# Kernel tuning notes

Measured on AMD Instinct MI355X. Metric: run time of the kernel, lower is better.

Reference implementation:

```python
import jax, jax.numpy as jnp
import numpy as np

HID = 1024
NH = 16
HD = HID // NH  # 64
RANK = 16
B, L = 2, 2048


def setup_inputs() -> dict:
    key = jax.random.key(0)
    ks = jax.random.split(key, 9)
    s = 0.02
    return {
        "x": jax.random.normal(ks[0], (B, L, HID), dtype=jnp.float32),
        "Wq": jax.random.normal(ks[1], (HID, HID), dtype=jnp.float32) * s,
        "Wk": jax.random.normal(ks[2], (HID, HID), dtype=jnp.float32) * s,
        "Wv": jax.random.normal(ks[3], (HID, HID), dtype=jnp.float32) * s,
        "Wg": jax.random.normal(ks[4], (HID, HID), dtype=jnp.float32) * s,
        "Wgk1": jax.random.normal(ks[5], (HID, RANK), dtype=jnp.float32) * s,
        "Wgk2": jax.random.normal(ks[6], (RANK, HID), dtype=jnp.float32) * s,
        "bgk2": jnp.zeros((HID,), dtype=jnp.float32),
        "gamma": jnp.ones((HID,), dtype=jnp.float32),
        "beta": jnp.zeros((HID,), dtype=jnp.float32),
        "Wout": jax.random.normal(ks[7], (HID, HID), dtype=jnp.float32) * s,
    }


def reference(x, Wq, Wk, Wv, Wg, Wgk1, Wgk2, bgk2, gamma, beta, Wout):
    Bb, Ll, Hid = x.shape
    H, Dh = NH, HD
    # projections -> [B, L, H, Dh]
    q = (x @ Wq).reshape(Bb, Ll, H, Dh)
    k = (x @ Wk).reshape(Bb, Ll, H, Dh)
    v = (x @ Wv).reshape(Bb, Ll, H, Dh)
    gk = (jax.nn.log_sigmoid((x @ Wgk1) @ Wgk2 + bgk2) / 16.0).reshape(Bb, Ll, H, Dh)

    # time-major for scan: [L, B, H, Dh]
    qT = jnp.transpose(q, (1, 0, 2, 3))
    kT = jnp.transpose(k, (1, 0, 2, 3))
    vT = jnp.transpose(v, (1, 0, 2, 3))
    gT = jnp.transpose(gk, (1, 0, 2, 3))

    def step(state, inp):
        qt, kt, vt, gt = inp  # each [B, H, Dh]
        gate = jnp.exp(gt)
        # state[b,h,v_dim,k_dim]; gate applied along v_dim (matches torch code)
        state = state * gate[..., None] + vt[..., None] * kt[..., None, :]
        out_t = jnp.einsum('bhvk,bhk->bhv', state, qt)
        return state, out_t

    state0 = jnp.zeros((Bb, H, Dh, Dh), dtype=x.dtype)
    _, outs = jax.lax.scan(step, state0, (qT, kT, vT, gT))  # outs: [L, B, H, Dh]
    out = jnp.transpose(outs, (1, 0, 2, 3)).reshape(Bb, Ll, Hid)

    # LayerNorm over total_dim
    mu = out.mean(-1, keepdims=True)
    var = out.var(-1, keepdims=True)
    out = (out - mu) / jnp.sqrt(var + 1e-5) * gamma + beta

    # output gate + projection (dropout = identity in eval)
    out = out * jax.nn.silu(x @ Wg)
    return out @ Wout
```

## Files before the change

### kernel.cpp

```cpp
#include <hip/hip_runtime.h>
#include <cstdint>
#include <cstddef>

#define HIDS 1024
#define NHEAD 16
#define HDIM 64
#define LSEQ 2048
#define BBATCH 2
#define NROW (BBATCH * LSEQ)
#define CHUNK 64
#define NCHUNK (LSEQ / CHUNK)
#define RANK 16

typedef short short8 __attribute__((ext_vector_type(8)));
typedef float floatx4 __attribute__((ext_vector_type(4)));

__device__ __forceinline__ ushort f2bf(float f) {
  uint32_t u = __float_as_uint(f);
  uint32_t r = (u + 0x7fffu + ((u >> 16) & 1u)) >> 16;
  return (ushort)r;
}
__device__ __forceinline__ float bf2f(ushort u) {
  return __uint_as_float(((uint32_t)u) << 16);
}
__device__ __forceinline__ float logsig16(float z) {
  return (fminf(z, 0.f) - __logf(1.f + __expf(-fabsf(z)))) * (1.f / 16.f);
}

__device__ __forceinline__ void async_copy16(const void* g, void* l) {
  __builtin_amdgcn_global_load_lds(
      (const __attribute__((address_space(1))) void*)g,
      (__attribute__((address_space(3))) void*)l, 16, 0, 0);
}

__global__ __launch_bounds__(256) void prep_kernel(
    const float* __restrict__ x, ushort* __restrict__ xbf,
    const float* __restrict__ W0, const float* __restrict__ W1,
    const float* __restrict__ W2, const float* __restrict__ W3,
    const float* __restrict__ W4, ushort* __restrict__ T0,
    ushort* __restrict__ T1, ushort* __restrict__ T2, ushort* __restrict__ T3,
    ushort* __restrict__ T4, const float* __restrict__ Wgk1,
    const float* __restrict__ Wgk2, ushort* __restrict__ Wte) {
  __shared__ float sbuf[64 * 65];
  const int bid = blockIdx.x;
  const int tid = threadIdx.x;

  if (bid < 4096) {
    const int i = bid * 256 + tid;
    float4 f = *(const float4*)(x + (size_t)i * 4);
    ushort4 o;
    o.x = f2bf(f.x); o.y = f2bf(f.y); o.z = f2bf(f.z); o.w = f2bf(f.w);
    *(ushort4*)(xbf + (size_t)i * 4) = o;
  } else if (bid < 5376) {
    const int w = bid - 4096;
    const int z = w >> 8, rem = w & 255;
    const float* W = (z == 0) ? W0 : (z == 1) ? W1 : (z == 2) ? W2
                     : (z == 3) ? W3 : W4;
    ushort* T = (z == 0) ? T0 : (z == 1) ? T1 : (z == 2) ? T2
                : (z == 3) ? T3 : T4;
    const int k0 = (rem >> 4) * 64, n0 = (rem & 15) * 64;
    const int r = tid >> 2, c4 = (tid & 3) * 16;
#pragma unroll
    for (int i = 0; i < 4; ++i) {
      float4 f = *(const float4*)(W + (size_t)(k0 + r) * HIDS + n0 + c4 + i * 4);
      sbuf[r * 65 + c4 + i * 4 + 0] = f.x;
      sbuf[r * 65 + c4 + i * 4 + 1] = f.y;
      sbuf[r * 65 + c4 + i * 4 + 2] = f.z;
      sbuf[r * 65 + c4 + i * 4 + 3] = f.w;
    }
    __syncthreads();
    const int n = tid >> 2, kc = (tid & 3) * 16;
#pragma unroll
    for (int i = 0; i < 4; ++i) {
      int kk = kc + i * 4;
      ushort4 o;
      o.x = f2bf(sbuf[(kk + 0) * 65 + n]);
      o.y = f2bf(sbuf[(kk + 1) * 65 + n]);
      o.z = f2bf(sbuf[(kk + 2) * 65 + n]);
      o.w = f2bf(sbuf[(kk + 3) * 65 + n]);
      *(ushort4*)(T + (size_t)(n0 + n) * HIDS + k0 + kk) = o;
    }
  } else {
    const int rem = bid - 5376;
    const int n0 = (rem & 15) * 64, k0 = (rem >> 4) * 64;
    float* sW1 = sbuf;
    float* sW2 = sbuf + 64 * 17;
    {
      const int kl = tid >> 2, r4 = (tid & 3) * 4;
      float4 f = *(const float4*)(Wgk1 + (size_t)(k0 + kl) * RANK + r4);
      sW1[kl * 17 + r4] = f.x; sW1[kl * 17 + r4 + 1] = f.y;
      sW1[kl * 17 + r4 + 2] = f.z; sW1[kl * 17 + r4 + 3] = f.w;
      const int rr = tid >> 4, nl = (tid & 15) * 4;
      float4 g = *(const float4*)(Wgk2 + (size_t)rr * HIDS + n0 + nl);
      sW2[rr * 65 + nl] = g.x; sW2[rr * 65 + nl + 1] = g.y;
      sW2[rr * 65 + nl + 2] = g.z; sW2[rr * 65 + nl + 3] = g.w;
    }
    __syncthreads();
    const int nl = tid & 63, kq = (tid >> 6) * 16;
    float w2[16];
#pragma unroll
    for (int r = 0; r < 16; ++r) w2[r] = sW2[r * 65 + nl];
    ushort ob[16];
#pragma unroll
    for (int i = 0; i < 16; ++i) {
      float s = 0.f;
#pragma unroll
      for (int r = 0; r < 16; ++r) s = fmaf(sW1[(kq + i) * 17 + r], w2[r], s);
      ob[i] = f2bf(s);
    }
#pragma unroll
    for (int i = 0; i < 2; ++i)
      *(short8*)(Wte + (size_t)(n0 + nl) * HIDS + k0 + kq + i * 8) =
          *(short8*)&ob[i * 8];
  }
}

__global__ __launch_bounds__(256) void proj5_kernel(
    const ushort* __restrict__ xbf, const ushort* __restrict__ Wtq,
    const ushort* __restrict__ Wtk, const ushort* __restrict__ Wtv,
    const ushort* __restrict__ Wtg, const ushort* __restrict__ Wte,
    ushort* __restrict__ qb, ushort* __restrict__ kb, ushort* __restrict__ vb,
    ushort* __restrict__ gb, ushort* __restrict__ zb) {
  const int bxz = blockIdx.x;
  const int z = bxz % 5;
  const int bx = bxz / 5;
  const ushort* Bt = (z == 0) ? Wtq : (z == 1) ? Wtk : (z == 2) ? Wtv
                     : (z == 3) ? Wtg : Wte;
  ushort* C = (z == 0) ? qb : (z == 1) ? kb : (z == 2) ? vb : (z == 3) ? gb : zb;
  __shared__ ushort As[2][128 * 32];
  __shared__ ushort Bs[2][128 * 32];
  const int tid = threadIdx.x;
  const int wave = tid >> 6, lane = tid & 63;
  const int wm = (wave >> 1) * 64, wn = (wave & 1) * 64;
  const int bm = blockIdx.y * 128, bn = bx * 128;
  const int lrow = tid >> 2;
  const int lk8 = ((((tid & 3) - ((tid >> 3) & 3)) & 3)) * 8;
  const ushort* Ag = xbf + (size_t)(bm + lrow) * HIDS + lk8;
  const ushort* Bg = Bt + (size_t)(bn + lrow) * HIDS + lk8;
  char* A0 = (char*)&As[0][0] + tid * 16;
  char* A1 = (char*)&As[1][0] + tid * 16;
  char* B0 = (char*)&Bs[0][0] + tid * 16;
  char* B1 = (char*)&Bs[1][0] + tid * 16;

  floatx4 acc[4][4];
#pragma unroll
  for (int i = 0; i < 4; ++i)
#pragma unroll
    for (int j = 0; j < 4; ++j) acc[i][j] = (floatx4){0.f, 0.f, 0.f, 0.f};

  const int fm = lane & 15, quad = lane >> 4;
  const int sq8 = ((quad + (fm >> 1)) & 3) * 8;

  for (int k0 = 0; k0 < HIDS; k0 += 64) {
    __syncthreads();
    async_copy16(Ag + k0, A0);
    async_copy16(Ag + (size_t)64 * HIDS + k0, A0 + 4096);
    async_copy16(Ag + k0 + 32, A1);
    async_copy16(Ag + (size_t)64 * HIDS + k0 + 32, A1 + 4096);
    async_copy16(Bg + k0, B0);
    async_copy16(Bg + (size_t)64 * HIDS + k0, B0 + 4096);
    async_copy16(Bg + k0 + 32, B1);
    async_copy16(Bg + (size_t)64 * HIDS + k0 + 32, B1 + 4096);
    __syncthreads();

#pragma unroll
    for (int ks = 0; ks < 2; ++ks) {
      short8 af[4], bfr[4];
#pragma unroll
      for (int i = 0; i < 4; ++i)
        af[i] = *(const short8*)&As[ks][(wm + i * 16 + fm) * 32 + sq8];
#pragma unroll
      for (int j = 0; j < 4; ++j)
        bfr[j] = *(const short8*)&Bs[ks][(wn + j * 16 + fm) * 32 + sq8];
#pragma unroll
      for (int i = 0; i < 4; ++i)
#pragma unroll
        for (int j = 0; j < 4; ++j)
          acc[i][j] = __builtin_amdgcn_mfma_f32_16x16x32_bf16(af[i], bfr[j],
                                                              acc[i][j], 0, 0, 0);
    }
  }

#pragma unroll
  for (int i = 0; i < 4; ++i) {
    const int row0 = bm + wm + i * 16 + quad * 4;
#pragma unroll
    for (int j = 0; j < 4; ++j) {
      const int col = bn + wn + j * 16 + fm;
#pragma unroll
      for (int r = 0; r < 4; ++r)
        C[(size_t)(row0 + r) * HIDS + col] = f2bf(acc[i][j][r]);
    }
  }
}

__global__ __launch_bounds__(256) void gemm_out_kernel(
    const ushort* __restrict__ A, const ushort* __restrict__ Bt,
    float* __restrict__ C) {
  __shared__ ushort As[2][128 * 32];
  __shared__ ushort Bs[2][64 * 32];
  const int tid = threadIdx.x;
  const int wave = tid >> 6, lane = tid & 63;
  const int fm = lane & 15, quad = lane >> 4;
  const int sq8 = ((quad + (fm >> 1)) & 3) * 8;
  const int bm = blockIdx.y * 128, bn = blockIdx.x * 64;
  const int lrow = tid >> 2;
  const int lk8 = ((((tid & 3) - ((tid >> 3) & 3)) & 3)) * 8;
  const ushort* Ag = A + (size_t)(bm + lrow) * HIDS + lk8;
  const ushort* Bg = Bt + (size_t)(bn + lrow) * HIDS + lk8;
  char* A0 = (char*)&As[0][0] + tid * 16;
  char* A1 = (char*)&As[1][0] + tid * 16;
  char* B0 = (char*)&Bs[0][0] + tid * 16;
  char* B1 = (char*)&Bs[1][0] + tid * 16;

  floatx4 acc[2][4];
#pragma unroll
  for (int i = 0; i < 2; ++i)
#pragma unroll
    for (int j = 0; j < 4; ++j) acc[i][j] = (floatx4){0.f, 0.f, 0.f, 0.f};

  for (int k0 = 0; k0 < HIDS; k0 += 64) {
    __syncthreads();
    async_copy16(Ag + k0, A0);
    async_copy16(Ag + (size_t)64 * HIDS + k0, A0 + 4096);
    async_copy16(Ag + k0 + 32, A1);
    async_copy16(Ag + (size_t)64 * HIDS + k0 + 32, A1 + 4096);
    async_copy16(Bg + k0, B0);
    async_copy16(Bg + k0 + 32, B1);
    __syncthreads();

#pragma unroll
    for (int ks = 0; ks < 2; ++ks) {
      short8 af[2], bfr[4];
#pragma unroll
      for (int i = 0; i < 2; ++i)
        af[i] = *(const short8*)&As[ks][(wave * 32 + i * 16 + fm) * 32 + sq8];
#pragma unroll
      for (int j = 0; j < 4; ++j)
        bfr[j] = *(const short8*)&Bs[ks][(j * 16 + fm) * 32 + sq8];
#pragma unroll
      for (int i = 0; i < 2; ++i)
#pragma unroll
        for (int j = 0; j < 4; ++j)
          acc[i][j] = __builtin_amdgcn_mfma_f32_16x16x32_bf16(af[i], bfr[j],
                                                              acc[i][j], 0, 0, 0);
    }
  }

#pragma unroll
  for (int i = 0; i < 2; ++i) {
    const int row0 = bm + wave * 32 + i * 16 + quad * 4;
#pragma unroll
    for (int j = 0; j < 4; ++j) {
      const int col = bn + j * 16 + fm;
#pragma unroll
      for (int r = 0; r < 4; ++r)
        C[(size_t)(row0 + r) * HIDS + col] = acc[i][j][r];
    }
  }
}

#define SP 72
#define SGS 68

__global__ __launch_bounds__(256) void sdelta_kernel(
    const ushort* __restrict__ k, const ushort* __restrict__ v,
    const ushort* __restrict__ zb, const float* __restrict__ bgk2,
    ushort* __restrict__ Sdelta, float* __restrict__ Lam,
    ushort* __restrict__ Vtg, ushort* __restrict__ Eb) {
  const int bid = blockIdx.x;
  const int c = bid & 31, bh = bid >> 5;
  const int b = bh >> 4, h = bh & 15;
  const int tid = threadIdx.x;
  const int lane = tid & 63, wave = tid >> 6;
  const int fm = lane & 15, quad = lane >> 4;
  const int wm2 = (wave >> 1) * 32, wn2 = (wave & 1) * 32;

  __shared__ ushort sKt[64 * SP];
  __shared__ ushort sVt[64 * SP];
  __shared__ float sG[64 * SGS];

  const size_t base = ((size_t)b * LSEQ + (size_t)c * CHUNK) * HIDS + (size_t)h * HDIM;
  const int r = tid >> 2, c0 = (tid & 3) * 16;
  const size_t gb = base + (size_t)r * HIDS + c0;
  {
    float bias[16];
#pragma unroll
    for (int m = 0; m < 4; ++m)
      *(float4*)&bias[m * 4] = *(const float4*)(bgk2 + h * HDIM + c0 + m * 4);
    short8 z0 = *(const short8*)(zb + gb);
    short8 z1 = *(const short8*)(zb + gb + 8);
#pragma unroll
    for (int i = 0; i < 16; ++i) {
      float zz = bf2f((ushort)(i < 8 ? z0[i] : z1[i - 8])) + bias[i];
      sG[r * SGS + c0 + i] = logsig16(zz);
    }
  }
  const int pr = (tid >> 3) * 2, pc = (tid & 7) * 8;
  const size_t pb = base + (size_t)pr * HIDS + pc;
  short8 ka = *(const short8*)(k + pb);
  short8 kb2 = *(const short8*)(k + pb + HIDS);
  short8 va = *(const short8*)(v + pb);
  short8 vb2 = *(const short8*)(v + pb + HIDS);
  __syncthreads();

  const int vcol = tid & 63, qtr = tid >> 6;
  {
    float run = 0.f;
#pragma unroll
    for (int i = 0; i < 16; ++i) {
      int idx = (qtr * 16 + i) * SGS + vcol;
      run += sG[idx];
      sG[idx] = run;
    }
  }
  __syncthreads();
  float pre = 0.f;
  for (int j = 0; j < qtr; ++j) pre += sG[(j * 16 + 15) * SGS + vcol];
  __syncthreads();
#pragma unroll
  for (int i = 0; i < 16; ++i) sG[(qtr * 16 + i) * SGS + vcol] += pre;
  __syncthreads();

  {
    ushort eb[16];
#pragma unroll
    for (int i = 0; i < 16; ++i) eb[i] = f2bf(__expf(sG[r * SGS + c0 + i]));
    *(short8*)(Eb + gb) = *(short8*)&eb[0];
    *(short8*)(Eb + gb + 8) = *(short8*)&eb[8];
  }

#pragma unroll
  for (int i = 0; i < 8; ++i) {
    ushort2 kk;
    kk.x = (ushort)ka[i];
    kk.y = (ushort)kb2[i];
    *(ushort2*)&sKt[(pc + i) * SP + pr] = kk;
    float Ga = sG[pr * SGS + pc + i];
    float Gb2 = sG[(pr + 1) * SGS + pc + i];
    ushort2 vv;
    vv.x = f2bf(bf2f((ushort)va[i]) * __expf(-Ga));
    vv.y = f2bf(bf2f((ushort)vb2[i]) * __expf(-Gb2));
    *(ushort2*)&sVt[(pc + i) * SP + pr] = vv;
  }
  __syncthreads();

  {
    const size_t vb3 = (size_t)(bh * NCHUNK + c) * (HDIM * HDIM);
    *(short8*)(Vtg + vb3 + (size_t)r * HDIM + c0) = *(const short8*)&sVt[r * SP + c0];
    *(short8*)(Vtg + vb3 + (size_t)r * HDIM + c0 + 8) =
        *(const short8*)&sVt[r * SP + c0 + 8];
  }

  if (tid < 64)
    Lam[(size_t)(bh * NCHUNK + c) * HDIM + tid] = __expf(sG[63 * SGS + tid]);

  floatx4 accD[2][2];
#pragma unroll
  for (int i = 0; i < 2; ++i)
#pragma unroll
    for (int j = 0; j < 2; ++j) accD[i][j] = (floatx4){0.f, 0.f, 0.f, 0.f};
#pragma unroll
  for (int ks = 0; ks < 2; ++ks) {
    short8 av[2], bk[2];
#pragma unroll
    for (int i = 0; i < 2; ++i)
      av[i] = *(const short8*)&sVt[(wm2 + i * 16 + fm) * SP + ks * 32 + quad * 8];
#pragma unroll
    for (int j = 0; j < 2; ++j)
      bk[j] = *(const short8*)&sKt[(wn2 + j * 16 + fm) * SP + ks * 32 + quad * 8];
#pragma unroll
    for (int i = 0; i < 2; ++i)
#pragma unroll
      for (int j = 0; j < 2; ++j)
        accD[i][j] = __builtin_amdgcn_mfma_f32_16x16x32_bf16(av[i], bk[j],
                                                             accD[i][j], 0, 0, 0);
  }
  const size_t sbase = (size_t)(bh * NCHUNK + c) * (HDIM * HDIM);
#pragma unroll
  for (int i = 0; i < 2; ++i) {
    const int m0 = wm2 + i * 16 + quad * 4;
    float lam[4];
#pragma unroll
    for (int rr = 0; rr < 4; ++rr) lam[rr] = __expf(sG[63 * SGS + m0 + rr]);
#pragma unroll
    for (int j = 0; j < 2; ++j) {
      const int n = wn2 + j * 16 + fm;
#pragma unroll
      for (int rr = 0; rr < 4; ++rr)
        Sdelta[sbase + (size_t)(m0 + rr) * HDIM + n] = f2bf(accD[i][j][rr] * lam[rr]);
    }
  }
}

__global__ __launch_bounds__(256) void state_scan_kernel(
    const ushort* __restrict__ Sdelta, const float* __restrict__ Lam,
    ushort* __restrict__ Sprev) {
  const int bh = blockIdx.x >> 3;
  const int sl = blockIdx.x & 7;
  const int tid = threadIdx.x;
  const int e0 = sl * 512 + tid;
  float S0 = 0.f, S1 = 0.f;

  float pd0[2], pd1[2], pl0[2], pl1[2];
#pragma unroll
  for (int s = 0; s < 2; ++s) {
    size_t nb = (size_t)(bh * NCHUNK + s) * (HDIM * HDIM);
    size_t nl = (size_t)(bh * NCHUNK + s) * HDIM;
    pd0[s] = bf2f(Sdelta[nb + e0]);
    pd1[s] = bf2f(Sdelta[nb + e0 + 256]);
    pl0[s] = Lam[nl + (e0 >> 6)];
    pl1[s] = Lam[nl + ((e0 + 256) >> 6)];
  }

  for (int c = 0; c < NCHUNK; ++c) {
    const int s = c & 1;
    float cd0 = pd0[s], cd1 = pd1[s], cl0 = pl0[s], cl1 = pl1[s];
    if (c + 2 < NCHUNK) {
      size_t nb = (size_t)(bh * NCHUNK + c + 2) * (HDIM * HDIM);
      size_t nl = (size_t)(bh * NCHUNK + c + 2) * HDIM;
      pd0[s] = bf2f(Sdelta[nb + e0]);
      pd1[s] = bf2f(Sdelta[nb + e0 + 256]);
      pl0[s] = Lam[nl + (e0 >> 6)];
      pl1[s] = Lam[nl + ((e0 + 256) >> 6)];
    }
    size_t ob = (size_t)(bh * NCHUNK + c) * (HDIM * HDIM);
    Sprev[ob + e0] = f2bf(S0);
    Sprev[ob + e0 + 256] = f2bf(S1);
    S0 = fmaf(S0, cl0, cd0);
    S1 = fmaf(S1, cl1, cd1);
  }
}

__global__ __launch_bounds__(256) void chunk_fused_kernel(
    const ushort* __restrict__ q, const ushort* __restrict__ k,
    const ushort* __restrict__ Vtg, const ushort* __restrict__ Eb,
    const ushort* __restrict__ Sprev, ushort* __restrict__ att) {
  const int bid = blockIdx.x;
  const int c = bid & 31, bh = bid >> 5;
  const int b = bh >> 4, h = bh & 15;
  const int tid = threadIdx.x;
  const int lane = tid & 63, wave = tid >> 6;
  const int fm = lane & 15, quad = lane >> 4;
  const int wm2 = (wave >> 1) * 32, wn2 = (wave & 1) * 32;

  __shared__ ushort sQ[64 * SP];
  __shared__ ushort sK[64 * SP];
  __shared__ ushort sVt[64 * SP];
  __shared__ ushort sA[64 * SP];
  ushort* sSp = sK;

  const size_t base = ((size_t)b * LSEQ + (size_t)c * CHUNK) * HIDS + (size_t)h * HDIM;
  const size_t sbase = (size_t)(bh * NCHUNK + c) * (HDIM * HDIM);
  const int r = tid >> 2, c0 = (tid & 3) * 16;
  const size_t gb = base + (size_t)r * HIDS + c0;
  short8 sp0 = *(const short8*)(Sprev + sbase + (size_t)r * HDIM + c0);
  short8 sp1 = *(const short8*)(Sprev + sbase + (size_t)r * HDIM + c0 + 8);
  *(short8*)&sQ[r * SP + c0] = *(const short8*)(q + gb);
  *(short8*)&sQ[r * SP + c0 + 8] = *(const short8*)(q + gb + 8);
  *(short8*)&sK[r * SP + c0] = *(const short8*)(k + gb);
  *(short8*)&sK[r * SP + c0 + 8] = *(const short8*)(k + gb + 8);
  *(short8*)&sVt[r * SP + c0] = *(const short8*)(Vtg + sbase + (size_t)r * HDIM + c0);
  *(short8*)&sVt[r * SP + c0 + 8] =
      *(const short8*)(Vtg + sbase + (size_t)r * HDIM + c0 + 8);
  __syncthreads();

  floatx4 accS[2][2];
#pragma unroll
  for (int i = 0; i < 2; ++i)
#pragma unroll
    for (int j = 0; j < 2; ++j) accS[i][j] = (floatx4){0.f, 0.f, 0.f, 0.f};
#pragma unroll
  for (int ks = 0; ks < 2; ++ks) {
    short8 a[2], bb[2];
#pragma unroll
    for (int i = 0; i < 2; ++i)
      a[i] = *(const short8*)&sQ[(wm2 + i * 16 + fm) * SP + ks * 32 + quad * 8];
#pragma unroll
    for (int j = 0; j < 2; ++j)
      bb[j] = *(const short8*)&sK[(wn2 + j * 16 + fm) * SP + ks * 32 + quad * 8];
#pragma unroll
    for (int i = 0; i < 2; ++i)
#pragma unroll
      for (int j = 0; j < 2; ++j)
        accS[i][j] = __builtin_amdgcn_mfma_f32_16x16x32_bf16(a[i], bb[j],
                                                             accS[i][j], 0, 0, 0);
  }
  __syncthreads();

#pragma unroll
  for (int i = 0; i < 2; ++i)
#pragma unroll
    for (int j = 0; j < 2; ++j) {
      const int t0 = wm2 + i * 16 + quad * 4;
      const int s = wn2 + j * 16 + fm;
#pragma unroll
      for (int rr = 0; rr < 4; ++rr) {
        float val = (s <= t0 + rr) ? accS[i][j][rr] : 0.f;
        sA[(t0 + rr) * SP + s] = f2bf(val);
      }
    }
  *(short8*)&sSp[r * SP + c0] = sp0;
  *(short8*)&sSp[r * SP + c0 + 8] = sp1;
  __syncthreads();

  floatx4 acc[2][2];
#pragma unroll
  for (int i = 0; i < 2; ++i)
#pragma unroll
    for (int j = 0; j < 2; ++j) acc[i][j] = (floatx4){0.f, 0.f, 0.f, 0.f};
#pragma unroll
  for (int ks = 0; ks < 2; ++ks) {
    short8 aa[2], aq[2], bv[2], bs[2];
#pragma unroll
    for (int i = 0; i < 2; ++i) {
      aa[i] = *(const short8*)&sA[(wm2 + i * 16 + fm) * SP + ks * 32 + quad * 8];
      aq[i] = *(const short8*)&sQ[(wm2 + i * 16 + fm) * SP + ks * 32 + quad * 8];
    }
#pragma unroll
    for (int j = 0; j < 2; ++j) {
      bv[j] = *(const short8*)&sVt[(wn2 + j * 16 + fm) * SP + ks * 32 + quad * 8];
      bs[j] = *(const short8*)&sSp[(wn2 + j * 16 + fm) * SP + ks * 32 + quad * 8];
    }
#pragma unroll
    for (int i = 0; i < 2; ++i)
#pragma unroll
      for (int j = 0; j < 2; ++j) {
        acc[i][j] = __builtin_amdgcn_mfma_f32_16x16x32_bf16(aa[i], bv[j],
                                                            acc[i][j], 0, 0, 0);
        acc[i][j] = __builtin_amdgcn_mfma_f32_16x16x32_bf16(aq[i], bs[j],
                                                            acc[i][j], 0, 0, 0);
      }
  }
#pragma unroll
  for (int i = 0; i < 2; ++i)
#pragma unroll
    for (int j = 0; j < 2; ++j) {
      const int m0 = wm2 + i * 16 + quad * 4;
      const int n = wn2 + j * 16 + fm;
#pragma unroll
      for (int rr = 0; rr < 4; ++rr) {
        const size_t idx = base + (size_t)(m0 + rr) * HIDS + n;
        att[idx] = f2bf(acc[i][j][rr] * bf2f(Eb[idx]));
      }
    }
}

__global__ __launch_bounds__(256) void ln_gate_kernel(const ushort* __restrict__ att,
                                                      const ushort* __restrict__ g,
                                                      const float* __restrict__ gamma,
                                                      const float* __restrict__ beta,
                                                      ushort* __restrict__ ybf) {
  const int row = blockIdx.x;
  const int tid = threadIdx.x;
  ushort4 au = *(const ushort4*)(att + (size_t)row * HIDS + tid * 4);
  float ax = bf2f(au.x), ay = bf2f(au.y), az = bf2f(au.z), aw = bf2f(au.w);
  float s = ax + ay + az + aw;
  float ss = ax * ax + ay * ay + az * az + aw * aw;
#pragma unroll
  for (int off = 32; off; off >>= 1) {
    s += __shfl_down(s, off);
    ss += __shfl_down(ss, off);
  }
  __shared__ float rs[4], rss[4];
  const int wid = tid >> 6;
  if ((tid & 63) == 0) { rs[wid] = s; rss[wid] = ss; }
  __syncthreads();
  const float mean = (rs[0] + rs[1] + rs[2] + rs[3]) * (1.f / HIDS);
  const float ex2 = (rss[0] + rss[1] + rss[2] + rss[3]) * (1.f / HIDS);
  const float rstd = rsqrtf(ex2 - mean * mean + 1e-5f);

  float4 ga = *(const float4*)(gamma + tid * 4);
  float4 be = *(const float4*)(beta + tid * 4);
  ushort4 gu = *(const ushort4*)(g + (size_t)row * HIDS + tid * 4);
  float gx = bf2f(gu.x), gy = bf2f(gu.y), gz = bf2f(gu.z), gw = bf2f(gu.w);
  float4 o;
  o.x = ((ax - mean) * rstd * ga.x + be.x) * (gx / (1.f + __expf(-gx)));
  o.y = ((ay - mean) * rstd * ga.y + be.y) * (gy / (1.f + __expf(-gy)));
  o.z = ((az - mean) * rstd * ga.z + be.z) * (gz / (1.f + __expf(-gz)));
  o.w = ((aw - mean) * rstd * ga.w + be.w) * (gw / (1.f + __expf(-gw)));
  ushort4 ob;
  ob.x = f2bf(o.x); ob.y = f2bf(o.y); ob.z = f2bf(o.z); ob.w = f2bf(o.w);
  *(ushort4*)(ybf + (size_t)row * HIDS + tid * 4) = ob;
}

extern "C" void kernel_launch(void* const* d_in, const int* in_sizes, int n_in,
                              void* d_out, int out_size, void* d_ws, size_t ws_size,
                              hipStream_t stream) {
  const float* x     = (const float*)d_in[0];
  const float* Wq    = (const float*)d_in[1];
  const float* Wk    = (const float*)d_in[2];
  const float* Wv    = (const float*)d_in[3];
  const float* Wg    = (const float*)d_in[4];
  const float* Wgk1  = (const float*)d_in[5];
  const float* Wgk2  = (const float*)d_in[6];
  const float* bgk2  = (const float*)d_in[7];
  const float* gamma = (const float*)d_in[8];
  const float* beta  = (const float*)d_in[9];
  const float* Wout  = (const float*)d_in[10];
  float* out = (float*)d_out;

  const size_t SZ = (size_t)NROW * HIDS;
  float* ws = (float*)d_ws;
  float* Lamb = ws;
  ushort* attb   = (ushort*)(ws + 65536);
  ushort* Sdelta = attb + SZ;
  ushort* Sprevb = Sdelta + SZ;
  ushort* Vtgb   = Sprevb + SZ;
  ushort* Ebb    = Vtgb + SZ;
  ushort* qbf = Ebb + SZ;
  ushort* kbf = qbf + SZ;
  ushort* vbf = kbf + SZ;
  ushort* gbf = vbf + SZ;
  ushort* zbf = gbf + SZ;
  ushort* xbf = zbf + SZ;
  ushort* Wtq = xbf + SZ;
  ushort* Wtk = Wtq + HIDS * HIDS;
  ushort* Wtv = Wtk + HIDS * HIDS;
  ushort* Wtg = Wtv + HIDS * HIDS;
  ushort* Wto = Wtg + HIDS * HIDS;
  ushort* Wte = Wto + HIDS * HIDS;
  ushort* ybf = vbf;

  prep_kernel<<<4096 + 1280 + 256, 256, 0, stream>>>(
      x, xbf, Wq, Wk, Wv, Wg, Wout, Wtq, Wtk, Wtv, Wtg, Wto, Wgk1, Wgk2, Wte);

  proj5_kernel<<<dim3(5 * (HIDS / 128), NROW / 128), 256, 0, stream>>>(
      xbf, Wtq, Wtk, Wtv, Wtg, Wte, qbf, kbf, vbf, gbf, zbf);

  sdelta_kernel<<<BBATCH * NHEAD * NCHUNK, 256, 0, stream>>>(
      kbf, vbf, zbf, bgk2, Sdelta, Lamb, Vtgb, Ebb);
  state_scan_kernel<<<256, 256, 0, stream>>>(Sdelta, Lamb, Sprevb);
  chunk_fused_kernel<<<BBATCH * NHEAD * NCHUNK, 256, 0, stream>>>(
      qbf, kbf, Vtgb, Ebb, Sprevb, attb);

  ln_gate_kernel<<<NROW, 256, 0, stream>>>(attb, gbf, gamma, beta, ybf);
  gemm_out_kernel<<<dim3(HIDS / 64, NROW / 128), 256, 0, stream>>>(ybf, Wto, out);
}
```

Baseline: 211.8 us.

## Replace dense low-rank gate projection with rank-16 factorized path and widen output GEMM tile

Drops the precomputed dense Wgk1·Wgk2 weight and its fifth 1024x1024 projection GEMM. A new small kernel computes x·Wgk1 (rank 16) in fp32, and sdelta expands it per head with Wgk2 in registers before the log-sigmoid. This removes about a fifth of the projection FLOPs and one bf16 intermediate buffer, and the gate logits are now computed in fp32 rather than through a bf16 product. The output GEMM also moves from 128x64 to 128x128 tiles with a 2x2 wave layout, trading fewer blocks for more reuse per block.

```diff
diff --git a/kernel.cpp b/kernel.cpp
--- a/kernel.cpp
+++ b/kernel.cpp
@@ -39,8 +39,7 @@
     const float* __restrict__ W2, const float* __restrict__ W3,
     const float* __restrict__ W4, ushort* __restrict__ T0,
     ushort* __restrict__ T1, ushort* __restrict__ T2, ushort* __restrict__ T3,
-    ushort* __restrict__ T4, const float* __restrict__ Wgk1,
-    const float* __restrict__ Wgk2, ushort* __restrict__ Wte) {
+    ushort* __restrict__ T4) {
   __shared__ float sbuf[64 * 65];
   const int bid = blockIdx.x;
   const int tid = threadIdx.x;
@@ -51,7 +50,7 @@
     ushort4 o;
     o.x = f2bf(f.x); o.y = f2bf(f.y); o.z = f2bf(f.z); o.w = f2bf(f.w);
     *(ushort4*)(xbf + (size_t)i * 4) = o;
-  } else if (bid < 5376) {
+  } else {
     const int w = bid - 4096;
     const int z = w >> 8, rem = w & 255;
     const float* W = (z == 0) ? W0 : (z == 1) ? W1 : (z == 2) ? W2
@@ -80,53 +79,51 @@
       o.w = f2bf(sbuf[(kk + 3) * 65 + n]);
       *(ushort4*)(T + (size_t)(n0 + n) * HIDS + k0 + kk) = o;
     }
-  } else {
-    const int rem = bid - 5376;
-    const int n0 = (rem & 15) * 64, k0 = (rem >> 4) * 64;
-    float* sW1 = sbuf;
-    float* sW2 = sbuf + 64 * 17;
-    {
-      const int kl = tid >> 2, r4 = (tid & 3) * 4;
-      float4 f = *(const float4*)(Wgk1 + (size_t)(k0 + kl) * RANK + r4);
-      sW1[kl * 17 + r4] = f.x; sW1[kl * 17 + r4 + 1] = f.y;
-      sW1[kl * 17 + r4 + 2] = f.z; sW1[kl * 17 + r4 + 3] = f.w;
-      const int rr = tid >> 4, nl = (tid & 15) * 4;
-      float4 g = *(const float4*)(Wgk2 + (size_t)rr * HIDS + n0 + nl);
-      sW2[rr * 65 + nl] = g.x; sW2[rr * 65 + nl + 1] = g.y;
-      sW2[rr * 65 + nl + 2] = g.z; sW2[rr * 65 + nl + 3] = g.w;
-    }
-    __syncthreads();
-    const int nl = tid & 63, kq = (tid >> 6) * 16;
-    float w2[16];
-#pragma unroll
-    for (int r = 0; r < 16; ++r) w2[r] = sW2[r * 65 + nl];
-    ushort ob[16];
-#pragma unroll
-    for (int i = 0; i < 16; ++i) {
-      float s = 0.f;
-#pragma unroll
-      for (int r = 0; r < 16; ++r) s = fmaf(sW1[(kq + i) * 17 + r], w2[r], s);
-      ob[i] = f2bf(s);
-    }
-#pragma unroll
-    for (int i = 0; i < 2; ++i)
-      *(short8*)(Wte + (size_t)(n0 + nl) * HIDS + k0 + kq + i * 8) =
-          *(short8*)&ob[i * 8];
-  }
-}
-
-__global__ __launch_bounds__(256) void proj5_kernel(
+  }
+}
+
+#define XSTR 1040
+__global__ __launch_bounds__(256) void xr_kernel(
+    const ushort* __restrict__ xbf, const float* __restrict__ Wgk1,
+    float* __restrict__ xr) {
+  __shared__ float sW1[HIDS * RANK];
+  __shared__ ushort sX[16 * XSTR];
+  const int tid = threadIdx.x;
+  const int r0 = blockIdx.x * 16;
+#pragma unroll
+  for (int j = 0; j < 16; ++j) {
+    const int idx = j * 1024 + tid * 4;
+    *(float4*)&sW1[idx] = *(const float4*)(Wgk1 + idx);
+  }
+#pragma unroll
+  for (int j = 0; j < 8; ++j) {
+    const int e = j * 2048 + tid * 8;
+    const int rr = e >> 10, kk = e & 1023;
+    *(short8*)&sX[rr * XSTR + kk] =
+        *(const short8*)(xbf + (size_t)(r0 + rr) * HIDS + kk);
+  }
+  __syncthreads();
+  const int r = tid >> 4, n = tid & 15;
+  float acc = 0.f;
+  for (int k8 = 0; k8 < HIDS; k8 += 8) {
+    short8 xv = *(const short8*)&sX[r * XSTR + k8];
+#pragma unroll
+    for (int i = 0; i < 8; ++i)
+      acc = fmaf(bf2f((ushort)xv[i]), sW1[(k8 + i) * RANK + n], acc);
+  }
+  xr[(size_t)(r0 + r) * RANK + n] = acc;
+}
+
+__global__ __launch_bounds__(256) void proj4_kernel(
     const ushort* __restrict__ xbf, const ushort* __restrict__ Wtq,
     const ushort* __restrict__ Wtk, const ushort* __restrict__ Wtv,
-    const ushort* __restrict__ Wtg, const ushort* __restrict__ Wte,
-    ushort* __restrict__ qb, ushort* __restrict__ kb, ushort* __restrict__ vb,
-    ushort* __restrict__ gb, ushort* __restrict__ zb) {
+    const ushort* __restrict__ Wtg, ushort* __restrict__ qb,
+    ushort* __restrict__ kb, ushort* __restrict__ vb, ushort* __restrict__ gb) {
   const int bxz = blockIdx.x;
-  const int z = bxz % 5;
-  const int bx = bxz / 5;
-  const ushort* Bt = (z == 0) ? Wtq : (z == 1) ? Wtk : (z == 2) ? Wtv
-                     : (z == 3) ? Wtg : Wte;
-  ushort* C = (z == 0) ? qb : (z == 1) ? kb : (z == 2) ? vb : (z == 3) ? gb : zb;
+  const int z = bxz & 3;
+  const int bx = bxz >> 2;
+  const ushort* Bt = (z == 0) ? Wtq : (z == 1) ? Wtk : (z == 2) ? Wtv : Wtg;
+  ushort* C = (z == 0) ? qb : (z == 1) ? kb : (z == 2) ? vb : gb;
   __shared__ ushort As[2][128 * 32];
   __shared__ ushort Bs[2][128 * 32];
   const int tid = threadIdx.x;
@@ -198,12 +195,13 @@
     const ushort* __restrict__ A, const ushort* __restrict__ Bt,
     float* __restrict__ C) {
   __shared__ ushort As[2][128 * 32];
-  __shared__ ushort Bs[2][64 * 32];
+  __shared__ ushort Bs[2][128 * 32];
   const int tid = threadIdx.x;
   const int wave = tid >> 6, lane = tid & 63;
+  const int wm = (wave >> 1) * 64, wn = (wave & 1) * 64;
   const int fm = lane & 15, quad = lane >> 4;
   const int sq8 = ((quad + (fm >> 1)) & 3) * 8;
-  const int bm = blockIdx.y * 128, bn = blockIdx.x * 64;
+  const int bm = blockIdx.y * 128, bn = blockIdx.x * 128;
   const int lrow = tid >> 2;
   const int lk8 = ((((tid & 3) - ((tid >> 3) & 3)) & 3)) * 8;
   const ushort* Ag = A + (size_t)(bm + lrow) * HIDS + lk8;
@@ -213,9 +211,9 @@
   char* B0 = (char*)&Bs[0][0] + tid * 16;
   char* B1 = (char*)&Bs[1][0] + tid * 16;
 
-  floatx4 acc[2][4];
-#pragma unroll
-  for (int i = 0; i < 2; ++i)
+  floatx4 acc[4][4];
+#pragma unroll
+  for (int i = 0; i < 4; ++i)
 #pragma unroll
     for (int j = 0; j < 4; ++j) acc[i][j] = (floatx4){0.f, 0.f, 0.f, 0.f};
 
@@ -226,20 +224,22 @@
     async_copy16(Ag + k0 + 32, A1);
     async_copy16(Ag + (size_t)64 * HIDS + k0 + 32, A1 + 4096);
     async_copy16(Bg + k0, B0);
+    async_copy16(Bg + (size_t)64 * HIDS + k0, B0 + 4096);
     async_copy16(Bg + k0 + 32, B1);
+    async_copy16(Bg + (size_t)64 * HIDS + k0 + 32, B1 + 4096);
     __syncthreads();
 
 #pragma unroll
     for (int ks = 0; ks < 2; ++ks) {
-      short8 af[2], bfr[4];
-#pragma unroll
-      for (int i = 0; i < 2; ++i)
-        af[i] = *(const short8*)&As[ks][(wave * 32 + i * 16 + fm) * 32 + sq8];
+      short8 af[4], bfr[4];
+#pragma unroll
+      for (int i = 0; i < 4; ++i)
+        af[i] = *(const short8*)&As[ks][(wm + i * 16 + fm) * 32 + sq8];
 #pragma unroll
       for (int j = 0; j < 4; ++j)
-        bfr[j] = *(const short8*)&Bs[ks][(j * 16 + fm) * 32 + sq8];
-#pragma unroll
-      for (int i = 0; i < 2; ++i)
+        bfr[j] = *(const short8*)&Bs[ks][(wn + j * 16 + fm) * 32 + sq8];
+#pragma unroll
+      for (int i = 0; i < 4; ++i)
 #pragma unroll
         for (int j = 0; j < 4; ++j)
           acc[i][j] = __builtin_amdgcn_mfma_f32_16x16x32_bf16(af[i], bfr[j],
@@ -248,11 +248,11 @@
   }
 
 #pragma unroll
-  for (int i = 0; i < 2; ++i) {
-    const int row0 = bm + wave * 32 + i * 16 + quad * 4;
+  for (int i = 0; i < 4; ++i) {
+    const int row0 = bm + wm + i * 16 + quad * 4;
 #pragma unroll
     for (int j = 0; j < 4; ++j) {
-      const int col = bn + j * 16 + fm;
+      const int col = bn + wn + j * 16 + fm;
 #pragma unroll
       for (int r = 0; r < 4; ++r)
         C[(size_t)(row0 + r) * HIDS + col] = acc[i][j][r];
@@ -265,9 +265,10 @@
 
 __global__ __launch_bounds__(256) void sdelta_kernel(
     const ushort* __restrict__ k, const ushort* __restrict__ v,
-    const ushort* __restrict__ zb, const float* __restrict__ bgk2,
-    ushort* __restrict__ Sdelta, float* __restrict__ Lam,
-    ushort* __restrict__ Vtg, ushort* __restrict__ Eb) {
+    const float* __restrict__ xr, const float* __restrict__ Wgk2,
+    const float* __restrict__ bgk2, ushort* __restrict__ Sdelta,
+    float* __restrict__ Lam, ushort* __restrict__ Vtg,
+    ushort* __restrict__ Eb) {
   const int bid = blockIdx.x;
   const int c = bid & 31, bh = bid >> 5;
   const int b = bh >> 4, h = bh & 15;
@@ -279,22 +280,37 @@
   __shared__ ushort sKt[64 * SP];
   __shared__ ushort sVt[64 * SP];
   __shared__ float sG[64 * SGS];
+  __shared__ float sW2[RANK * 64];
 
   const size_t base = ((size_t)b * LSEQ + (size_t)c * CHUNK) * HIDS + (size_t)h * HDIM;
   const int r = tid >> 2, c0 = (tid & 3) * 16;
   const size_t gb = base + (size_t)r * HIDS + c0;
+
   {
-    float bias[16];
+    const int wr = tid >> 4, wc = (tid & 15) * 4;
+    *(float4*)&sW2[wr * 64 + wc] =
+        *(const float4*)(Wgk2 + (size_t)wr * HIDS + h * HDIM + wc);
+  }
+  float xrr[16];
+  {
+    const size_t xrow = ((size_t)b * LSEQ + (size_t)c * CHUNK + r) * RANK;
 #pragma unroll
     for (int m = 0; m < 4; ++m)
-      *(float4*)&bias[m * 4] = *(const float4*)(bgk2 + h * HDIM + c0 + m * 4);
-    short8 z0 = *(const short8*)(zb + gb);
-    short8 z1 = *(const short8*)(zb + gb + 8);
-#pragma unroll
-    for (int i = 0; i < 16; ++i) {
-      float zz = bf2f((ushort)(i < 8 ? z0[i] : z1[i - 8])) + bias[i];
-      sG[r * SGS + c0 + i] = logsig16(zz);
-    }
+      *(float4*)&xrr[m * 4] = *(const float4*)(xr + xrow + m * 4);
+  }
+  float bias[16];
+#pragma unroll
+  for (int m = 0; m < 4; ++m)
+    *(float4*)&bias[m * 4] = *(const float4*)(bgk2 + h * HDIM + c0 + m * 4);
+  __syncthreads();
+
+#pragma unroll
+  for (int i = 0; i < 16; ++i) {
+    float z = bias[i];
+#pragma unroll
+    for (int t2 = 0; t2 < 16; ++t2)
+      z = fmaf(xrr[t2], sW2[t2 * 64 + c0 + i], z);
+    sG[r * SGS + c0 + i] = logsig16(z);
   }
   const int pr = (tid >> 3) * 2, pc = (tid & 7) * 8;
   const size_t pb = base + (size_t)pr * HIDS + pc;
@@ -612,28 +628,29 @@
   ushort* kbf = qbf + SZ;
   ushort* vbf = kbf + SZ;
   ushort* gbf = vbf + SZ;
-  ushort* zbf = gbf + SZ;
-  ushort* xbf = zbf + SZ;
+  ushort* xbf = gbf + SZ;
   ushort* Wtq = xbf + SZ;
   ushort* Wtk = Wtq + HIDS * HIDS;
   ushort* Wtv = Wtk + HIDS * HIDS;
   ushort* Wtg = Wtv + HIDS * HIDS;
   ushort* Wto = Wtg + HIDS * HIDS;
-  ushort* Wte = Wto + HIDS * HIDS;
+  float* xrb = (float*)(Wto + HIDS * HIDS);
   ushort* ybf = vbf;
 
-  prep_kernel<<<4096 + 1280 + 256, 256, 0, stream>>>(
-      x, xbf, Wq, Wk, Wv, Wg, Wout, Wtq, Wtk, Wtv, Wtg, Wto, Wgk1, Wgk2, Wte);
-
-  proj5_kernel<<<dim3(5 * (HIDS / 128), NROW / 128), 256, 0, stream>>>(
-      xbf, Wtq, Wtk, Wtv, Wtg, Wte, qbf, kbf, vbf, gbf, zbf);
+  prep_kernel<<<4096 + 1280, 256, 0, stream>>>(
+      x, xbf, Wq, Wk, Wv, Wg, Wout, Wtq, Wtk, Wtv, Wtg, Wto);
+
+  xr_kernel<<<NROW / 16, 256, 0, stream>>>(xbf, Wgk1, xrb);
+
+  proj4_kernel<<<dim3(4 * (HIDS / 128), NROW / 128), 256, 0, stream>>>(
+      xbf, Wtq, Wtk, Wtv, Wtg, qbf, kbf, vbf, gbf);
 
   sdelta_kernel<<<BBATCH * NHEAD * NCHUNK, 256, 0, stream>>>(
-      kbf, vbf, zbf, bgk2, Sdelta, Lamb, Vtgb, Ebb);
+      kbf, vbf, xrb, Wgk2, bgk2, Sdelta, Lamb, Vtgb, Ebb);
   state_scan_kernel<<<256, 256, 0, stream>>>(Sdelta, Lamb, Sprevb);
   chunk_fused_kernel<<<BBATCH * NHEAD * NCHUNK, 256, 0, stream>>>(
       qbf, kbf, Vtgb, Ebb, Sprevb, attb);
 
   ln_gate_kernel<<<NROW, 256, 0, stream>>>(attb, gbf, gamma, beta, ybf);
-  gemm_out_kernel<<<dim3(HIDS / 64, NROW / 128), 256, 0, stream>>>(ybf, Wto, out);
-}
+  gemm_out_kernel<<<dim3(HIDS / 128, NROW / 128), 256, 0, stream>>>(ybf, Wto, out);
+}
```

Result: slower. 222.8 us (+5.2%).
